# Performance work log

Hardware: AMD Instinct MI355X
Metric: run time of the kernel (lower is better)

## Reference

```python
import jax, jax.numpy as jnp
import numpy as np

B, N, C = 2, 30, 320
FH = FW = 64          # feature map (latent 128 / downsample 2)
PH = PW = 32          # roi_scale output size at this level
ORIG = 128.0          # original (latent) spatial size
SCALE = 0.5           # spatial_scale = 1/downsample_rate
SR = 2                # sampling_ratio
M = N + 1             # global channel + rois


def _bilinear(img, y, x):
    # img: (C, H, W); y, x: arbitrary-shape float coords. torchvision-style:
    # zero outside [-1, H]/[ -1, W], clamp then 4-corner interp.
    H, W = img.shape[1], img.shape[2]
    valid = (y > -1.0) & (y < H) & (x > -1.0) & (x < W)
    yc = jnp.clip(y, 0.0, H - 1.0)
    xc = jnp.clip(x, 0.0, W - 1.0)
    y0 = jnp.floor(yc).astype(jnp.int32)
    x0 = jnp.floor(xc).astype(jnp.int32)
    y1 = jnp.minimum(y0 + 1, H - 1)
    x1 = jnp.minimum(x0 + 1, W - 1)
    wy = yc - y0
    wx = xc - x0
    v = (img[:, y0, x0] * (1 - wy) * (1 - wx)
         + img[:, y0, x1] * (1 - wy) * wx
         + img[:, y1, x0] * wy * (1 - wx)
         + img[:, y1, x1] * wy * wx)
    return v * valid


def _roi_align_one(img, x1, y1, bw, bh):
    # img (C,FH,FW); x1,y1,bw,bh (N,) in aligned feature coords / bin sizes
    s = (jnp.arange(PH * SR, dtype=img.dtype) + 0.5) / SR   # sub-sample offsets in bin units
    yy = y1[:, None] + s[None, :] * bh[:, None]             # (N, PH*SR)
    xx = x1[:, None] + s[None, :] * bw[:, None]             # (N, PW*SR)
    yg = jnp.broadcast_to(yy[:, :, None], (N, PH * SR, PW * SR))
    xg = jnp.broadcast_to(xx[:, None, :], (N, PH * SR, PW * SR))
    v = _bilinear(img, yg, xg)                              # (C, N, PH*SR, PW*SR)
    v = v.reshape(C, N, PH, SR, PW, SR).mean(axis=(3, 5))   # average sub-samples
    return v.transpose(1, 0, 2, 3)                          # (N, C, PH, PW)


def _roi_unpool_one(roi_imgs, x1, y1, bw, bh):
    # inverse of roi_align: paste each (C,PH,PW) roi back into its own (FH,FW) map
    ys = jnp.arange(FH, dtype=roi_imgs.dtype)
    xs = jnp.arange(FW, dtype=roi_imgs.dtype)
    ry = (ys[None, :] - y1[:, None]) / bh[:, None] - 0.5    # (N, FH) roi-grid coords
    rx = (xs[None, :] - x1[:, None]) / bw[:, None] - 0.5    # (N, FW)
    ryg = jnp.broadcast_to(ry[:, :, None], (N, FH, FW))
    rxg = jnp.broadcast_to(rx[:, None, :], (N, FH, FW))
    return jax.vmap(_bilinear)(roi_imgs, ryg, rxg)          # (N, C, FH, FW); zeros outside box


def _fuser(x, perm, w_reduce, w1, b1, w2, b2):
    # FuseWeightGenerator: x (B, M, C, H, W)
    fg = jnp.sum(x, axis=2) != 0                            # (B, M, H, W) foreground mask
    fw = jnp.einsum('bmchw,c->bmhw', x, w_reduce)           # 1x1 conv C->1, no bias
    g = fw[:, :1]
    r = fw[:, 1:][:, perm]                                  # shuffle roi channels
    gin = jnp.concatenate([g, r], axis=1)                   # (B, M, H, W)
    # ChannelGate: only the 'max' branch affects the output (original uses last channel_att_raw)
    mp = gin.max(axis=(2, 3))                               # (B, M)
    att = jax.nn.relu(mp @ w1 + b1) @ w2 + b2
    gated = gin * jax.nn.sigmoid(att)[:, :, None, None]
    inv = jnp.argsort(perm)
    fw = jnp.concatenate([gated[:, :1], gated[:, 1:][:, inv]], axis=1)
    fw = jnp.where(fg, fw, jnp.finfo(fw.dtype).min)
    w = jax.nn.softmax(fw, axis=1)[:, :, None]              # (B, M, 1, H, W)
    return jnp.sum(x * w, axis=1)                           # (B, C, H, W)


def _forward(normed_hidden_states, attn_output, instance_boxes, instance_masks, perm,
             w_reduce, w1, b1, w2, b2):
    fmap = normed_hidden_states.reshape(B, FH, FW, C).transpose(0, 3, 1, 2)  # b c h w
    boxes = instance_boxes * ORIG * SCALE - 0.5             # aligned=True feature coords
    x1, y1 = boxes[..., 0], boxes[..., 1]
    x2, y2 = boxes[..., 2], boxes[..., 3]
    bw = (x2 - x1) / PW
    bh = (y2 - y1) / PH
    roi_feats = jax.vmap(_roi_align_one)(fmap, x1, y1, bw, bh)   # (B,N,C,PH,PW)
    mask = instance_masks.astype(roi_feats.dtype)[:, :, None, None, None]
    roi_feats = roi_feats * mask                             # masked rois stay zero
    unpooled = jax.vmap(_roi_unpool_one)(roi_feats, x1, y1, bw, bh) * mask  # (B,N,C,FH,FW)
    attn_map = attn_output.reshape(B, FH, FW, C).transpose(0, 3, 1, 2)[:, None]
    x = jnp.concatenate([attn_map, unpooled], axis=1)        # (B, M, C, FH, FW)
    fused = _fuser(x, perm, w_reduce, w1, b1, w2, b2)        # (B, C, FH, FW)
    return fused.transpose(0, 2, 3, 1).reshape(B, FH * FW, C)


def setup_inputs() -> dict:
    key = jax.random.key(0)
    ks = jax.random.split(key, 10)
    nhs = jax.random.normal(ks[0], (B, FH * FW, C), dtype=jnp.float32)
    attn = jax.random.normal(ks[1], (B, FH * FW, C), dtype=jnp.float32)
    cx = jax.random.uniform(ks[2], (B, N), minval=0.25, maxval=0.75)
    cy = jax.random.uniform(ks[3], (B, N), minval=0.25, maxval=0.75)
    hw = jax.random.uniform(ks[4], (B, N, 2), minval=0.1, maxval=0.4)
    boxes = jnp.stack([cx - hw[..., 0] / 2, cy - hw[..., 1] / 2,
                       cx + hw[..., 0] / 2, cy + hw[..., 1] / 2], axis=-1)
    boxes = jnp.clip(boxes, 0.0, 1.0).astype(jnp.float32)    # normalized xyxy
    masks = jax.random.randint(ks[5], (B, N), 0, 2).astype(jnp.int32)
    perm = jax.random.permutation(ks[6], N).astype(jnp.int32)
    w_reduce = (jax.random.normal(ks[7], (C,), dtype=jnp.float32) / np.sqrt(C)).astype(jnp.float32)
    w1 = (jax.random.normal(ks[8], (M, M), dtype=jnp.float32) / np.sqrt(M)).astype(jnp.float32)
    b1 = jnp.zeros((M,), dtype=jnp.float32)
    w2 = (jax.random.normal(ks[9], (M, M), dtype=jnp.float32) / np.sqrt(M)).astype(jnp.float32)
    b2 = jnp.zeros((M,), dtype=jnp.float32)
    return {"normed_hidden_states": nhs, "attn_output": attn, "instance_boxes": boxes,
            "instance_masks": masks, "perm": perm, "w_reduce": w_reduce,
            "w1": w1, "b1": b1, "w2": w2, "b2": b2}


def reference(normed_hidden_states, attn_output, instance_boxes, instance_masks, perm,
              w_reduce, w1, b1, w2, b2):
    return _forward(normed_hidden_states, attn_output, instance_boxes, instance_masks, perm,
                    w_reduce, w1, b1, w2, b2)
```

## Files before the change

kernel.cpp:

```cpp
#include <hip/hip_runtime.h>
#include <hip/hip_bf16.h>

#define NB 2
#define NN 30
#define NC 320
#define NM 31
#define HW 4096
#define FMIN_F (-3.40282346638528859812e+38f)

typedef float nfloat4 __attribute__((ext_vector_type(4)));

#define OFF_ASUM   0
#define OFF_AWRED  8192
#define OFF_RS     16384
#define OFF_RW     77824
#define OFF_MP     139264
#define WS_FLOATS  139328
#define ROIF_BYTE  557312

#define GRID_ROIF (NB * NN * 128)
#define GRID_RED  1639

__device__ __forceinline__ void get_box(const float* boxes, int b, int n,
                                        float& x1, float& y1, float& bw, float& bh) {
    const float* p = boxes + (b * NN + n) * 4;
    float X1 = p[0] * 64.0f - 0.5f;
    float Y1 = p[1] * 64.0f - 0.5f;
    float X2 = p[2] * 64.0f - 0.5f;
    float Y2 = p[3] * 64.0f - 0.5f;
    x1 = X1; y1 = Y1;
    bw = (X2 - X1) / 32.0f;
    bh = (Y2 - Y1) / 32.0f;
}

__device__ __forceinline__ unsigned short f2bf(float f) {
    __hip_bfloat16 h = __float2bfloat16(f);
    return *reinterpret_cast<unsigned short*>(&h);
}
__device__ __forceinline__ unsigned pack2(float a, float b) {
    return (unsigned)f2bf(a) | ((unsigned)f2bf(b) << 16);
}
__device__ __forceinline__ float blo(unsigned u) { return __uint_as_float(u << 16); }
__device__ __forceinline__ float bhi(unsigned u) { return __uint_as_float(u & 0xffff0000u); }

__device__ __forceinline__ unsigned encf(float f) {
    unsigned u = __float_as_uint(f);
    return (u & 0x80000000u) ? ~u : (u | 0x80000000u);
}
__device__ __forceinline__ float decf(unsigned e) {
    unsigned u = (e & 0x80000000u) ? (e & 0x7fffffffu) : ~e;
    return __uint_as_float(u);
}

__device__ void do_roifeat(int blk, const float* __restrict__ nhs,
                           const float* __restrict__ boxes,
                           const int* __restrict__ masks,
                           const float* __restrict__ wred,
                           float* __restrict__ ws,
                           unsigned* __restrict__ roif,
                           float* wsm , int* bsm ,
                           float* partS , float* partW ) {
    int bn = blk >> 7;
    int n = bn % NN;
    int b = bn / NN;
    if (masks[b * NN + n] == 0) return;
    int tid = threadIdx.x;
    float x1, y1, bw, bh;
    get_box(boxes, b, n, x1, y1, bw, bh);

    if (tid < 8) {
        int cell = blk * 8 + tid;
        int q = cell & 31;
        int p = (cell >> 5) & 31;
        float W[9] = {0.f,0.f,0.f,0.f,0.f,0.f,0.f,0.f,0.f};
        float wys[4], wxs[4];
        int iy0s[4], ix0s[4];
        int iymin = 64, ixmin = 64;
#pragma unroll
        for (int s_ = 0; s_ < 4; s_++) {
            int di = s_ >> 1, dj = s_ & 1;
            float y = y1 + ((float)p + 0.25f + 0.5f * (float)di) * bh;
            float x = x1 + ((float)q + 0.25f + 0.5f * (float)dj) * bw;
            float yc = fminf(fmaxf(y, 0.0f), 63.0f);
            float xc = fminf(fmaxf(x, 0.0f), 63.0f);
            int iy0 = (int)floorf(yc), ix0 = (int)floorf(xc);
            wys[s_] = yc - (float)iy0;
            wxs[s_] = xc - (float)ix0;
            iy0s[s_] = iy0; ix0s[s_] = ix0;
            iymin = min(iymin, iy0); ixmin = min(ixmin, ix0);
        }
#pragma unroll
        for (int s_ = 0; s_ < 4; s_++) {
            float wy = wys[s_], wx = wxs[s_];
            int dy = iy0s[s_] - iymin;
            int dx = ix0s[s_] - ixmin;
            bool yt = (iy0s[s_] == 63);
            bool xt = (ix0s[s_] == 63);
            float ay0 = yt ? 1.0f : (1.0f - wy);
            float ay1 = yt ? 0.0f : wy;
            float ax0 = xt ? 1.0f : (1.0f - wx);
            float ax1 = xt ? 0.0f : wx;
            float r0 = dy ? 0.0f : ay0;
            float r1 = dy ? ay0  : ay1;
            float r2 = dy ? ay1  : 0.0f;
            float c0 = dx ? 0.0f : ax0;
            float c1 = dx ? ax0  : ax1;
            float c2 = dx ? ax1  : 0.0f;
            W[0] += r0 * c0; W[1] += r0 * c1; W[2] += r0 * c2;
            W[3] += r1 * c0; W[4] += r1 * c1; W[5] += r1 * c2;
            W[6] += r2 * c0; W[7] += r2 * c1; W[8] += r2 * c2;
        }
#pragma unroll
        for (int k = 0; k < 9; k++) wsm[tid * 9 + k] = W[k] * 0.25f;
        bsm[tid] = iymin * 64 + ixmin;
    }
    __syncthreads();

    int cid = tid / 40;
    int v = tid - cid * 40;
    int cell = blk * 8 + cid;
    const float4* fb4 = (const float4*)(nhs + (size_t)b * HW * NC);
    int base = bsm[cid];
    float4 acc0 = make_float4(0.f, 0.f, 0.f, 0.f);
    float4 acc1 = make_float4(0.f, 0.f, 0.f, 0.f);
#pragma unroll
    for (int i = 0; i < 3; i++) {
#pragma unroll
        for (int j = 0; j < 3; j++) {
            float w = wsm[cid * 9 + i * 3 + j];
            if (w != 0.0f) {
                int off = (base + i * 64 + j) * 80 + v * 2;
                float4 f0 = fb4[off];
                float4 f1 = fb4[off + 1];
                acc0.x += w * f0.x; acc0.y += w * f0.y;
                acc0.z += w * f0.z; acc0.w += w * f0.w;
                acc1.x += w * f1.x; acc1.y += w * f1.y;
                acc1.z += w * f1.z; acc1.w += w * f1.w;
            }
        }
    }
    uint4 pk;
    pk.x = pack2(acc0.x, acc0.y);
    pk.y = pack2(acc0.z, acc0.w);
    pk.z = pack2(acc1.x, acc1.y);
    pk.w = pack2(acc1.z, acc1.w);
    ((uint4*)roif)[(size_t)cell * 40 + v] = pk;

    const float4* w4 = (const float4*)wred;
    float4 wv0 = w4[v * 2];
    float4 wv1 = w4[v * 2 + 1];
    partS[tid] = acc0.x + acc0.y + acc0.z + acc0.w + acc1.x + acc1.y + acc1.z + acc1.w;
    partW[tid] = acc0.x * wv0.x + acc0.y * wv0.y + acc0.z * wv0.z + acc0.w * wv0.w
               + acc1.x * wv1.x + acc1.y * wv1.y + acc1.z * wv1.z + acc1.w * wv1.w;
    __syncthreads();
    if (tid < 8) {
        float ss = 0.f, ww = 0.f;
#pragma unroll 8
        for (int k = 0; k < 40; k++) {
            ss += partS[tid * 40 + k];
            ww += partW[tid * 40 + k];
        }
        int c2 = blk * 8 + tid;
        ws[OFF_RS + c2] = ss;
        ws[OFF_RW + c2] = ww;
    }
}

__device__ void do_reduce(int rblk, const float* __restrict__ attn,
                          const float* __restrict__ wred, float* __restrict__ ws) {
    int wave = threadIdx.x >> 6;
    int lane = threadIdx.x & 63;
    int row = rblk * 5 + wave;
    if (row >= NB * HW) return;
    const float4* a4 = (const float4*)(attn + (size_t)row * NC);
    const float4* w4 = (const float4*)wred;
    float4 wv = w4[lane];
    float4 av = a4[lane];
    float s_a = av.x + av.y + av.z + av.w;
    float w_a = av.x * wv.x + av.y * wv.y + av.z * wv.z + av.w * wv.w;
    if (lane < 16) {
        float4 wv2 = w4[lane + 64];
        float4 av2 = a4[lane + 64];
        s_a += av2.x + av2.y + av2.z + av2.w;
        w_a += av2.x * wv2.x + av2.y * wv2.y + av2.z * wv2.z + av2.w * wv2.w;
    }
#pragma unroll
    for (int off = 32; off > 0; off >>= 1) {
        s_a += __shfl_down(s_a, off, 64);
        w_a += __shfl_down(w_a, off, 64);
    }
    if (lane == 0) {
        ws[OFF_ASUM + row]  = s_a;
        ws[OFF_AWRED + row] = w_a;
    }
}

__global__ void k_stage1(const float* __restrict__ nhs, const float* __restrict__ attn,
                         const float* __restrict__ boxes, const int* __restrict__ masks,
                         const float* __restrict__ wred, float* __restrict__ ws,
                         unsigned* __restrict__ roif) {
    __shared__ float wsm[72];
    __shared__ int bsm[8];
    __shared__ float partS[320], partW[320];
    int blk = blockIdx.x;
    if (blk < GRID_ROIF) {
        do_roifeat(blk, nhs, boxes, masks, wred, ws, roif, wsm, bsm, partS, partW);
    } else {
        do_reduce(blk - GRID_ROIF, attn, wred, ws);
    }
}

__global__ void k_fwmax(const float* __restrict__ boxes, const int* __restrict__ masks,
                        float* __restrict__ ws) {
    __shared__ float rwsm[1024];
    __shared__ float red[4];
    int tid = threadIdx.x;
    int bm = blockIdx.x;
    unsigned* MP = (unsigned*)(ws + OFF_MP);

    if (bm >= NB * NN) {
        int b = bm - NB * NN;
        const float* aw = ws + OFF_AWRED + b * HW;
        float lm = FMIN_F;
        for (int i = tid; i < HW; i += 256) lm = fmaxf(lm, aw[i]);
#pragma unroll
        for (int off = 32; off > 0; off >>= 1)
            lm = fmaxf(lm, __shfl_down(lm, off, 64));
        if ((tid & 63) == 0) red[tid >> 6] = lm;
        __syncthreads();
        if (tid == 0) {
            float mx = fmaxf(fmaxf(red[0], red[1]), fmaxf(red[2], red[3]));
            MP[b * NM] = encf(mx);
        }
        return;
    }

    int b = bm / NN, n = bm % NN;
    if (masks[b * NN + n] == 0) {
        if (tid == 0) MP[b * NM + 1 + n] = encf(0.0f);
        return;
    }
    const float* rw = ws + OFF_RW + (b * NN + n) * 1024;
    for (int i = tid; i < 1024; i += 256) rwsm[i] = rw[i];
    float x1, y1, bw, bh;
    get_box(boxes, b, n, x1, y1, bw, bh);
    __syncthreads();

    int h0  = max(0, (int)floorf(y1 - 0.5f * bh) - 1);
    int h1  = min(63, (int)ceilf(y1 + 32.5f * bh) + 1);
    int wq0 = max(0, (int)floorf(x1 - 0.5f * bw) - 1);
    int wq1 = min(63, (int)ceilf(x1 + 32.5f * bw) + 1);
    int Wd = wq1 - wq0 + 1;
    int tot = Wd * (h1 - h0 + 1);
    float lm = FMIN_F;
    for (int i = tid; i < tot; i += 256) {
        int h  = h0 + i / Wd;
        int wp = wq0 + i % Wd;
        float ry = ((float)h - y1) / bh - 0.5f;
        float rx = ((float)wp - x1) / bw - 0.5f;
        if (ry > -1.0f && ry < 32.0f && rx > -1.0f && rx < 32.0f) {
            float yc = fminf(fmaxf(ry, 0.0f), 31.0f);
            float xc = fminf(fmaxf(rx, 0.0f), 31.0f);
            int iy0 = (int)floorf(yc), ix0 = (int)floorf(xc);
            int iy1 = min(iy0 + 1, 31), ix1 = min(ix0 + 1, 31);
            float wy = yc - (float)iy0, wx = xc - (float)ix0;
            float fwv = (1.f - wy) * (1.f - wx) * rwsm[iy0 * 32 + ix0]
                      + (1.f - wy) * wx        * rwsm[iy0 * 32 + ix1]
                      + wy * (1.f - wx)        * rwsm[iy1 * 32 + ix0]
                      + wy * wx                * rwsm[iy1 * 32 + ix1];
            lm = fmaxf(lm, fwv);
        }
    }
#pragma unroll
    for (int off = 32; off > 0; off >>= 1)
        lm = fmaxf(lm, __shfl_down(lm, off, 64));
    if ((tid & 63) == 0) red[tid >> 6] = lm;
    __syncthreads();
    if (tid == 0) {
        float mx = fmaxf(fmaxf(red[0], red[1]), fmaxf(red[2], red[3]));
        MP[b * NM + 1 + n] = encf(fmaxf(mx, 0.0f));
    }
}

__global__ void k_final(const float* __restrict__ attn, const float* __restrict__ boxes,
                        const int* __restrict__ masks, const int* __restrict__ perm,
                        const float* __restrict__ w1, const float* __restrict__ b1,
                        const float* __restrict__ w2, const float* __restrict__ b2,
                        const float* __restrict__ ws, const unsigned* __restrict__ roif,
                        float* __restrict__ out) {
    __shared__ float mpg[NM], hb[NM], scal[32], wbuf[8][32];
    __shared__ int acnt[8];
    __shared__ unsigned char alist[8][NN];
    int t = threadIdx.x;
    int idx0 = blockIdx.x * 8;
    int b = idx0 >> 12;

    if (t < 8) acnt[t] = 0;
    if (t < NM) {
        unsigned e = ((const unsigned*)(ws + OFF_MP))[b * NM + ((t == 0) ? 0 : 1 + perm[t - 1])];
        mpg[t] = decf(e);
    }
    __syncthreads();
    if (t < NM) {
        float a = b1[t];
#pragma unroll
        for (int k = 0; k < NM; k++) a += mpg[k] * w1[k * NM + t];
        hb[t] = fmaxf(a, 0.0f);
    }
    __syncthreads();
    if (t < NM) {
        float a = b2[t];
#pragma unroll
        for (int k = 0; k < NM; k++) a += hb[k] * w2[k * NM + t];
        float sig = 1.0f / (1.0f + expf(-a));
        if (t == 0) scal[0] = sig;
        else        scal[1 + perm[t - 1]] = sig;
    }
    __syncthreads();

    if (t < 256) {
        int pg = t >> 5, m = t & 31;
        int pix = (idx0 + pg) & 4095;
        float zz = FMIN_F;
        if (m == 0) {
            float fwv = ws[OFF_AWRED + b * HW + pix];
            bool fg = (ws[OFF_ASUM + b * HW + pix] != 0.0f);
            zz = fg ? fwv * scal[0] : FMIN_F;
        } else if (m < NM) {
            int n = m - 1;
            if (masks[b * NN + n]) {
                float x1, y1, bw, bh;
                get_box(boxes, b, n, x1, y1, bw, bh);
                int h = pix >> 6, wp = pix & 63;
                float ry = ((float)h - y1) / bh - 0.5f;
                float rx = ((float)wp - x1) / bw - 0.5f;
                bool valid = (ry > -1.0f) && (ry < 32.0f) && (rx > -1.0f) && (rx < 32.0f);
                if (valid) {
                    float yc = fminf(fmaxf(ry, 0.0f), 31.0f);
                    float xc = fminf(fmaxf(rx, 0.0f), 31.0f);
                    int iy0 = (int)floorf(yc), ix0 = (int)floorf(xc);
                    int iy1 = min(iy0 + 1, 31), ix1 = min(ix0 + 1, 31);
                    float wy = yc - (float)iy0, wx = xc - (float)ix0;
                    float w00 = (1.f - wy) * (1.f - wx), w01 = (1.f - wy) * wx;
                    float w10 = wy * (1.f - wx), w11 = wy * wx;
                    const float* rw = ws + OFF_RW + (b * NN + n) * 1024;
                    const float* rs = ws + OFF_RS + (b * NN + n) * 1024;
                    float fwv = w00 * rw[iy0 * 32 + ix0] + w01 * rw[iy0 * 32 + ix1]
                              + w10 * rw[iy1 * 32 + ix0] + w11 * rw[iy1 * 32 + ix1];
                    float su  = w00 * rs[iy0 * 32 + ix0] + w01 * rs[iy0 * 32 + ix1]
                              + w10 * rs[iy1 * 32 + ix0] + w11 * rs[iy1 * 32 + ix1];
                    if (su != 0.0f) zz = fwv * scal[m];
                }
            }
        }
        float mx = zz;
#pragma unroll
        for (int off = 16; off > 0; off >>= 1)
            mx = fmaxf(mx, __shfl_xor(mx, off, 64));
        float e = (m < NM) ? expf(zz - mx) : 0.0f;
        float s = e;
#pragma unroll
        for (int off = 16; off > 0; off >>= 1)
            s += __shfl_xor(s, off, 64);
        if (m < NM) {
            float w = e / s;
            wbuf[pg][m] = w;
            if (m >= 1 && w != 0.0f) {
                int pos = atomicAdd(&acnt[pg], 1);
                alist[pg][pos] = (unsigned char)(m - 1);
            }
        }
    }
    __syncthreads();

    int pid = t / 40;
    int v = t - pid * 40;
    int idx = idx0 + pid;
    int pix = idx & 4095;
    int h = pix >> 6, wp = pix & 63;
    float w0 = wbuf[pid][0];
    const float4* at4 = (const float4*)attn;
    float4 a0 = at4[(size_t)idx * 80 + v * 2];
    float4 a1 = at4[(size_t)idx * 80 + v * 2 + 1];
    float4 acc0, acc1;
    acc0.x = a0.x * w0; acc0.y = a0.y * w0; acc0.z = a0.z * w0; acc0.w = a0.w * w0;
    acc1.x = a1.x * w0; acc1.y = a1.y * w0; acc1.z = a1.z * w0; acc1.w = a1.w * w0;
    const uint4* r4 = (const uint4*)roif;
    int na = acnt[pid];
    for (int k = 0; k < na; k++) {
        int n = alist[pid][k];
        float wn = wbuf[pid][n + 1];
        float x1, y1, bw, bh;
        get_box(boxes, b, n, x1, y1, bw, bh);
        float ry = ((float)h - y1) / bh - 0.5f;
        float rx = ((float)wp - x1) / bw - 0.5f;
        float yc = fminf(fmaxf(ry, 0.0f), 31.0f);
        float xc = fminf(fmaxf(rx, 0.0f), 31.0f);
        int iy0 = (int)floorf(yc), ix0 = (int)floorf(xc);
        int iy1 = min(iy0 + 1, 31), ix1 = min(ix0 + 1, 31);
        float wy = yc - (float)iy0, wx = xc - (float)ix0;
        float w00 = (1.f - wy) * (1.f - wx) * wn, w01 = (1.f - wy) * wx * wn;
        float w10 = wy * (1.f - wx) * wn, w11 = wy * wx * wn;
        size_t base = ((size_t)(b * NN + n)) << 10;
        uint4 U00 = r4[(base + iy0 * 32 + ix0) * 40 + v];
        uint4 U01 = r4[(base + iy0 * 32 + ix1) * 40 + v];
        uint4 U10 = r4[(base + iy1 * 32 + ix0) * 40 + v];
        uint4 U11 = r4[(base + iy1 * 32 + ix1) * 40 + v];
        acc0.x += w00 * blo(U00.x) + w01 * blo(U01.x) + w10 * blo(U10.x) + w11 * blo(U11.x);
        acc0.y += w00 * bhi(U00.x) + w01 * bhi(U01.x) + w10 * bhi(U10.x) + w11 * bhi(U11.x);
        acc0.z += w00 * blo(U00.y) + w01 * blo(U01.y) + w10 * blo(U10.y) + w11 * blo(U11.y);
        acc0.w += w00 * bhi(U00.y) + w01 * bhi(U01.y) + w10 * bhi(U10.y) + w11 * bhi(U11.y);
        acc1.x += w00 * blo(U00.z) + w01 * blo(U01.z) + w10 * blo(U10.z) + w11 * blo(U11.z);
        acc1.y += w00 * bhi(U00.z) + w01 * bhi(U01.z) + w10 * bhi(U10.z) + w11 * bhi(U11.z);
        acc1.z += w00 * blo(U00.w) + w01 * blo(U01.w) + w10 * blo(U10.w) + w11 * blo(U11.w);
        acc1.w += w00 * bhi(U00.w) + w01 * bhi(U01.w) + w10 * bhi(U10.w) + w11 * bhi(U11.w);
    }
    nfloat4 nv0 = { acc0.x, acc0.y, acc0.z, acc0.w };
    nfloat4 nv1 = { acc1.x, acc1.y, acc1.z, acc1.w };
    __builtin_nontemporal_store(nv0, ((nfloat4*)out) + (size_t)idx * 80 + v * 2);
    __builtin_nontemporal_store(nv1, ((nfloat4*)out) + (size_t)idx * 80 + v * 2 + 1);
}

extern "C" void kernel_launch(void* const* d_in, const int* in_sizes, int n_in,
                              void* d_out, int out_size, void* d_ws, size_t ws_size,
                              hipStream_t stream) {
    const float* nhs   = (const float*)d_in[0];
    const float* attn  = (const float*)d_in[1];
    const float* boxes = (const float*)d_in[2];
    const int*   masks = (const int*)d_in[3];
    const int*   perm  = (const int*)d_in[4];
    const float* wred  = (const float*)d_in[5];
    const float* w1    = (const float*)d_in[6];
    const float* b1    = (const float*)d_in[7];
    const float* w2    = (const float*)d_in[8];
    const float* b2    = (const float*)d_in[9];
    float* out = (float*)d_out;
    float* ws = (float*)d_ws;
    unsigned* roif = (unsigned*)((char*)d_ws + ROIF_BYTE);

    k_stage1<<<GRID_ROIF + GRID_RED, 320, 0, stream>>>(nhs, attn, boxes, masks, wred, ws, roif);
    k_fwmax<<<NB * NN + NB, 256, 0, stream>>>(boxes, masks, ws);
    k_final<<<NB * HW / 8, 320, 0, stream>>>(attn, boxes, masks, perm, w1, b1, w2, b2, ws, roif, out);
}
```

Baseline: 119.6 us.

## Drop materialized ROI feature maps; compose align+unpool weights directly on nhs

Removes the bf16 ROI-aligned feature buffer (B*N*1024 cells x 320 channels). The per-ROI channel sum and weighted sum are now computed from per-pixel reductions of nhs, since the reduction is linear, so only a 64x64 scalar grid needs resampling. In the final kernel the roi_align and unpool bilinear weights are composed into a separable 4x4 stencil applied to nhs directly. This removes a large write and read of intermediate data and the bf16 rounding, at the cost of up to 16 instead of 4 gathers per active ROI per pixel in the final pass.

Result: slower. 123.5 us (+3.3%).

```diff
diff --git a/kernel.cpp b/kernel.cpp
--- a/kernel.cpp
+++ b/kernel.cpp
@@ -1,5 +1,4 @@
 #include <hip/hip_runtime.h>
-#include <hip/hip_bf16.h>
 
 #define NB 2
 #define NN 30
@@ -12,14 +11,13 @@
 
 #define OFF_ASUM   0
 #define OFF_AWRED  8192
-#define OFF_RS     16384
-#define OFF_RW     77824
-#define OFF_MP     139264
-#define WS_FLOATS  139328
-#define ROIF_BYTE  557312
-
-#define GRID_ROIF (NB * NN * 128)
-#define GRID_RED  1639
+#define OFF_GS     16384
+#define OFF_GW     24576
+#define OFF_RS     32768
+#define OFF_RW     94208
+#define OFF_MP     155648
+
+#define GRID_RED 3277
 
 __device__ __forceinline__ void get_box(const float* boxes, int b, int n,
                                         float& x1, float& y1, float& bw, float& bh) {
@@ -33,16 +31,6 @@
     bh = (Y2 - Y1) / 32.0f;
 }
 
-__device__ __forceinline__ unsigned short f2bf(float f) {
-    __hip_bfloat16 h = __float2bfloat16(f);
-    return *reinterpret_cast<unsigned short*>(&h);
-}
-__device__ __forceinline__ unsigned pack2(float a, float b) {
-    return (unsigned)f2bf(a) | ((unsigned)f2bf(b) << 16);
-}
-__device__ __forceinline__ float blo(unsigned u) { return __uint_as_float(u << 16); }
-__device__ __forceinline__ float bhi(unsigned u) { return __uint_as_float(u & 0xffff0000u); }
-
 __device__ __forceinline__ unsigned encf(float f) {
     unsigned u = __float_as_uint(f);
     return (u & 0x80000000u) ? ~u : (u | 0x80000000u);
@@ -52,26 +40,92 @@
     return __uint_as_float(u);
 }
 
-__device__ void do_roifeat(int blk, const float* __restrict__ nhs,
-                           const float* __restrict__ boxes,
-                           const int* __restrict__ masks,
-                           const float* __restrict__ wred,
-                           float* __restrict__ ws,
-                           unsigned* __restrict__ roif,
-                           float* wsm , int* bsm ,
-                           float* partS , float* partW ) {
-    int bn = blk >> 7;
-    int n = bn % NN;
-    int b = bn / NN;
-    if (masks[b * NN + n] == 0) return;
+__global__ void k_reduce(const float* __restrict__ nhs, const float* __restrict__ attn,
+                         const float* __restrict__ wred, float* __restrict__ ws) {
+    int wave = threadIdx.x >> 6;
+    int lane = threadIdx.x & 63;
+    int row = blockIdx.x * 5 + wave;
+    if (row >= 2 * NB * HW) return;
+    const float* src;
+    float *d0, *d1;
+    if (row < NB * HW) {
+        src = attn + (size_t)row * NC;
+        d0 = ws + OFF_ASUM + row;
+        d1 = ws + OFF_AWRED + row;
+    } else {
+        int r = row - NB * HW;
+        src = nhs + (size_t)r * NC;
+        d0 = ws + OFF_GS + r;
+        d1 = ws + OFF_GW + r;
+    }
+    const float4* a4 = (const float4*)src;
+    const float4* w4 = (const float4*)wred;
+    float4 wv = w4[lane];
+    float4 av = a4[lane];
+    float s_a = av.x + av.y + av.z + av.w;
+    float w_a = av.x * wv.x + av.y * wv.y + av.z * wv.z + av.w * wv.w;
+    if (lane < 16) {
+        float4 wv2 = w4[lane + 64];
+        float4 av2 = a4[lane + 64];
+        s_a += av2.x + av2.y + av2.z + av2.w;
+        w_a += av2.x * wv2.x + av2.y * wv2.y + av2.z * wv2.z + av2.w * wv2.w;
+    }
+#pragma unroll
+    for (int off = 32; off > 0; off >>= 1) {
+        s_a += __shfl_down(s_a, off, 64);
+        w_a += __shfl_down(w_a, off, 64);
+    }
+    if (lane == 0) {
+        d0[0] = s_a;
+        d1[0] = w_a;
+    }
+}
+
+__global__ void k_grids(const float* __restrict__ boxes, const int* __restrict__ masks,
+                        float* __restrict__ ws) {
+    __shared__ float gsm[4096], gwm[4096];
+    __shared__ float rwsm[1024];
+    __shared__ float red[4];
     int tid = threadIdx.x;
+    int bm = blockIdx.x;
+    unsigned* MP = (unsigned*)(ws + OFF_MP);
+
+    if (bm >= NB * NN) {
+        int b = bm - NB * NN;
+        const float* aw = ws + OFF_AWRED + b * HW;
+        float lm = FMIN_F;
+        for (int i = tid; i < HW; i += 256) lm = fmaxf(lm, aw[i]);
+#pragma unroll
+        for (int off = 32; off > 0; off >>= 1)
+            lm = fmaxf(lm, __shfl_down(lm, off, 64));
+        if ((tid & 63) == 0) red[tid >> 6] = lm;
+        __syncthreads();
+        if (tid == 0) {
+            float mx = fmaxf(fmaxf(red[0], red[1]), fmaxf(red[2], red[3]));
+            MP[b * NM] = encf(mx);
+        }
+        return;
+    }
+
+    int b = bm / NN, n = bm % NN;
+    if (masks[b * NN + n] == 0) {
+        if (tid == 0) MP[b * NM + 1 + n] = encf(0.0f);
+        return;
+    }
+    const float* gs = ws + OFF_GS + b * HW;
+    const float* gw = ws + OFF_GW + b * HW;
+    for (int i = tid; i < 4096; i += 256) {
+        gsm[i] = gs[i];
+        gwm[i] = gw[i];
+    }
     float x1, y1, bw, bh;
     get_box(boxes, b, n, x1, y1, bw, bh);
-
-    if (tid < 8) {
-        int cell = blk * 8 + tid;
-        int q = cell & 31;
-        int p = (cell >> 5) & 31;
+    __syncthreads();
+
+    float* RS = ws + OFF_RS + (b * NN + n) * 1024;
+    float* RW = ws + OFF_RW + (b * NN + n) * 1024;
+    for (int c = tid; c < 1024; c += 256) {
+        int q = c & 31, p = c >> 5;
         float W[9] = {0.f,0.f,0.f,0.f,0.f,0.f,0.f,0.f,0.f};
         float wys[4], wxs[4];
         int iy0s[4], ix0s[4];
@@ -110,140 +164,21 @@
             W[3] += r1 * c0; W[4] += r1 * c1; W[5] += r1 * c2;
             W[6] += r2 * c0; W[7] += r2 * c1; W[8] += r2 * c2;
         }
-#pragma unroll
-        for (int k = 0; k < 9; k++) wsm[tid * 9 + k] = W[k] * 0.25f;
-        bsm[tid] = iymin * 64 + ixmin;
-    }
-    __syncthreads();
-
-    int cid = tid / 40;
-    int v = tid - cid * 40;
-    int cell = blk * 8 + cid;
-    const float4* fb4 = (const float4*)(nhs + (size_t)b * HW * NC);
-    int base = bsm[cid];
-    float4 acc0 = make_float4(0.f, 0.f, 0.f, 0.f);
-    float4 acc1 = make_float4(0.f, 0.f, 0.f, 0.f);
-#pragma unroll
-    for (int i = 0; i < 3; i++) {
-#pragma unroll
-        for (int j = 0; j < 3; j++) {
-            float w = wsm[cid * 9 + i * 3 + j];
-            if (w != 0.0f) {
-                int off = (base + i * 64 + j) * 80 + v * 2;
-                float4 f0 = fb4[off];
-                float4 f1 = fb4[off + 1];
-                acc0.x += w * f0.x; acc0.y += w * f0.y;
-                acc0.z += w * f0.z; acc0.w += w * f0.w;
-                acc1.x += w * f1.x; acc1.y += w * f1.y;
-                acc1.z += w * f1.z; acc1.w += w * f1.w;
+        int base = iymin * 64 + ixmin;
+        float ss = 0.f, ww = 0.f;
+#pragma unroll
+        for (int k = 0; k < 9; k++) {
+            if (W[k] != 0.0f) {
+                float wk = W[k] * 0.25f;
+                int off = base + (k / 3) * 64 + (k % 3);
+                ss += wk * gsm[off];
+                ww += wk * gwm[off];
             }
         }
-    }
-    uint4 pk;
-    pk.x = pack2(acc0.x, acc0.y);
-    pk.y = pack2(acc0.z, acc0.w);
-    pk.z = pack2(acc1.x, acc1.y);
-    pk.w = pack2(acc1.z, acc1.w);
-    ((uint4*)roif)[(size_t)cell * 40 + v] = pk;
-
-    const float4* w4 = (const float4*)wred;
-    float4 wv0 = w4[v * 2];
-    float4 wv1 = w4[v * 2 + 1];
-    partS[tid] = acc0.x + acc0.y + acc0.z + acc0.w + acc1.x + acc1.y + acc1.z + acc1.w;
-    partW[tid] = acc0.x * wv0.x + acc0.y * wv0.y + acc0.z * wv0.z + acc0.w * wv0.w
-               + acc1.x * wv1.x + acc1.y * wv1.y + acc1.z * wv1.z + acc1.w * wv1.w;
-    __syncthreads();
-    if (tid < 8) {
-        float ss = 0.f, ww = 0.f;
-#pragma unroll 8
-        for (int k = 0; k < 40; k++) {
-            ss += partS[tid * 40 + k];
-            ww += partW[tid * 40 + k];
-        }
-        int c2 = blk * 8 + tid;
-        ws[OFF_RS + c2] = ss;
-        ws[OFF_RW + c2] = ww;
-    }
-}
-
-__device__ void do_reduce(int rblk, const float* __restrict__ attn,
-                          const float* __restrict__ wred, float* __restrict__ ws) {
-    int wave = threadIdx.x >> 6;
-    int lane = threadIdx.x & 63;
-    int row = rblk * 5 + wave;
-    if (row >= NB * HW) return;
-    const float4* a4 = (const float4*)(attn + (size_t)row * NC);
-    const float4* w4 = (const float4*)wred;
-    float4 wv = w4[lane];
-    float4 av = a4[lane];
-    float s_a = av.x + av.y + av.z + av.w;
-    float w_a = av.x * wv.x + av.y * wv.y + av.z * wv.z + av.w * wv.w;
-    if (lane < 16) {
-        float4 wv2 = w4[lane + 64];
-        float4 av2 = a4[lane + 64];
-        s_a += av2.x + av2.y + av2.z + av2.w;
-        w_a += av2.x * wv2.x + av2.y * wv2.y + av2.z * wv2.z + av2.w * wv2.w;
-    }
-#pragma unroll
-    for (int off = 32; off > 0; off >>= 1) {
-        s_a += __shfl_down(s_a, off, 64);
-        w_a += __shfl_down(w_a, off, 64);
-    }
-    if (lane == 0) {
-        ws[OFF_ASUM + row]  = s_a;
-        ws[OFF_AWRED + row] = w_a;
-    }
-}
-
-__global__ void k_stage1(const float* __restrict__ nhs, const float* __restrict__ attn,
-                         const float* __restrict__ boxes, const int* __restrict__ masks,
-                         const float* __restrict__ wred, float* __restrict__ ws,
-                         unsigned* __restrict__ roif) {
-    __shared__ float wsm[72];
-    __shared__ int bsm[8];
-    __shared__ float partS[320], partW[320];
-    int blk = blockIdx.x;
-    if (blk < GRID_ROIF) {
-        do_roifeat(blk, nhs, boxes, masks, wred, ws, roif, wsm, bsm, partS, partW);
-    } else {
-        do_reduce(blk - GRID_ROIF, attn, wred, ws);
-    }
-}
-
-__global__ void k_fwmax(const float* __restrict__ boxes, const int* __restrict__ masks,
-                        float* __restrict__ ws) {
-    __shared__ float rwsm[1024];
-    __shared__ float red[4];
-    int tid = threadIdx.x;
-    int bm = blockIdx.x;
-    unsigned* MP = (unsigned*)(ws + OFF_MP);
-
-    if (bm >= NB * NN) {
-        int b = bm - NB * NN;
-        const float* aw = ws + OFF_AWRED + b * HW;
-        float lm = FMIN_F;
-        for (int i = tid; i < HW; i += 256) lm = fmaxf(lm, aw[i]);
-#pragma unroll
-        for (int off = 32; off > 0; off >>= 1)
-            lm = fmaxf(lm, __shfl_down(lm, off, 64));
-        if ((tid & 63) == 0) red[tid >> 6] = lm;
-        __syncthreads();
-        if (tid == 0) {
-            float mx = fmaxf(fmaxf(red[0], red[1]), fmaxf(red[2], red[3]));
-            MP[b * NM] = encf(mx);
-        }
-        return;
-    }
-
-    int b = bm / NN, n = bm % NN;
-    if (masks[b * NN + n] == 0) {
-        if (tid == 0) MP[b * NM + 1 + n] = encf(0.0f);
-        return;
-    }
-    const float* rw = ws + OFF_RW + (b * NN + n) * 1024;
-    for (int i = tid; i < 1024; i += 256) rwsm[i] = rw[i];
-    float x1, y1, bw, bh;
-    get_box(boxes, b, n, x1, y1, bw, bh);
+        RS[c] = ss;
+        RW[c] = ww;
+        rwsm[c] = ww;
+    }
     __syncthreads();
 
     int h0  = max(0, (int)floorf(y1 - 0.5f * bh) - 1);
@@ -282,12 +217,12 @@
     }
 }
 
-__global__ void k_final(const float* __restrict__ attn, const float* __restrict__ boxes,
-                        const int* __restrict__ masks, const int* __restrict__ perm,
+__global__ void k_final(const float* __restrict__ nhs, const float* __restrict__ attn,
+                        const float* __restrict__ boxes, const int* __restrict__ masks,
+                        const int* __restrict__ perm,
                         const float* __restrict__ w1, const float* __restrict__ b1,
                         const float* __restrict__ w2, const float* __restrict__ b2,
-                        const float* __restrict__ ws, const unsigned* __restrict__ roif,
-                        float* __restrict__ out) {
+                        const float* __restrict__ ws, float* __restrict__ out) {
     __shared__ float mpg[NM], hb[NM], scal[32], wbuf[8][32];
     __shared__ int acnt[8];
     __shared__ unsigned char alist[8][NN];
@@ -385,7 +320,7 @@
     float4 acc0, acc1;
     acc0.x = a0.x * w0; acc0.y = a0.y * w0; acc0.z = a0.z * w0; acc0.w = a0.w * w0;
     acc1.x = a1.x * w0; acc1.y = a1.y * w0; acc1.z = a1.z * w0; acc1.w = a1.w * w0;
-    const uint4* r4 = (const uint4*)roif;
+    const float4* fb4 = (const float4*)(nhs + (size_t)b * HW * NC);
     int na = acnt[pid];
     for (int k = 0; k < na; k++) {
         int n = alist[pid][k];
@@ -398,22 +333,60 @@
         float xc = fminf(fmaxf(rx, 0.0f), 31.0f);
         int iy0 = (int)floorf(yc), ix0 = (int)floorf(xc);
         int iy1 = min(iy0 + 1, 31), ix1 = min(ix0 + 1, 31);
-        float wy = yc - (float)iy0, wx = xc - (float)ix0;
-        float w00 = (1.f - wy) * (1.f - wx) * wn, w01 = (1.f - wy) * wx * wn;
-        float w10 = wy * (1.f - wx) * wn, w11 = wy * wx * wn;
-        size_t base = ((size_t)(b * NN + n)) << 10;
-        uint4 U00 = r4[(base + iy0 * 32 + ix0) * 40 + v];
-        uint4 U01 = r4[(base + iy0 * 32 + ix1) * 40 + v];
-        uint4 U10 = r4[(base + iy1 * 32 + ix0) * 40 + v];
-        uint4 U11 = r4[(base + iy1 * 32 + ix1) * 40 + v];
-        acc0.x += w00 * blo(U00.x) + w01 * blo(U01.x) + w10 * blo(U10.x) + w11 * blo(U11.x);
-        acc0.y += w00 * bhi(U00.x) + w01 * bhi(U01.x) + w10 * bhi(U10.x) + w11 * bhi(U11.x);
-        acc0.z += w00 * blo(U00.y) + w01 * blo(U01.y) + w10 * blo(U10.y) + w11 * blo(U11.y);
-        acc0.w += w00 * bhi(U00.y) + w01 * bhi(U01.y) + w10 * bhi(U10.y) + w11 * bhi(U11.y);
-        acc1.x += w00 * blo(U00.z) + w01 * blo(U01.z) + w10 * blo(U10.z) + w11 * blo(U11.z);
-        acc1.y += w00 * bhi(U00.z) + w01 * bhi(U01.z) + w10 * bhi(U10.z) + w11 * bhi(U11.z);
-        acc1.z += w00 * blo(U00.w) + w01 * blo(U01.w) + w10 * blo(U10.w) + w11 * blo(U11.w);
-        acc1.w += w00 * bhi(U00.w) + w01 * bhi(U01.w) + w10 * bhi(U10.w) + w11 * bhi(U11.w);
+        float fy = yc - (float)iy0, fx = xc - (float)ix0;
+
+        float ya00 = fminf(fmaxf(y1 + ((float)iy0 + 0.25f) * bh, 0.f), 63.f);
+        float ya01 = fminf(fmaxf(y1 + ((float)iy0 + 0.75f) * bh, 0.f), 63.f);
+        float ya10 = fminf(fmaxf(y1 + ((float)iy1 + 0.25f) * bh, 0.f), 63.f);
+        float ya11 = fminf(fmaxf(y1 + ((float)iy1 + 0.75f) * bh, 0.f), 63.f);
+        float xa00 = fminf(fmaxf(x1 + ((float)ix0 + 0.25f) * bw, 0.f), 63.f);
+        float xa01 = fminf(fmaxf(x1 + ((float)ix0 + 0.75f) * bw, 0.f), 63.f);
+        float xa10 = fminf(fmaxf(x1 + ((float)ix1 + 0.25f) * bw, 0.f), 63.f);
+        float xa11 = fminf(fmaxf(x1 + ((float)ix1 + 0.75f) * bw, 0.f), 63.f);
+        int rb = (int)floorf(ya00);
+        int cb = (int)floorf(xa00);
+        float wyv[4] = {0.f,0.f,0.f,0.f};
+        float wxv[4] = {0.f,0.f,0.f,0.f};
+        float cy0 = 0.5f * (1.0f - fy), cy1 = 0.5f * fy;
+        float cx0 = 0.5f * (1.0f - fx), cx1 = 0.5f * fx;
+        {
+            int i; float f;
+            i = (int)floorf(ya00); f = ya00 - (float)i;
+            wyv[i - rb] += cy0 * (1.f - f); wyv[min(i + 1, 63) - rb] += cy0 * f;
+            i = (int)floorf(ya01); f = ya01 - (float)i;
+            wyv[i - rb] += cy0 * (1.f - f); wyv[min(i + 1, 63) - rb] += cy0 * f;
+            i = (int)floorf(ya10); f = ya10 - (float)i;
+            wyv[i - rb] += cy1 * (1.f - f); wyv[min(i + 1, 63) - rb] += cy1 * f;
+            i = (int)floorf(ya11); f = ya11 - (float)i;
+            wyv[i - rb] += cy1 * (1.f - f); wyv[min(i + 1, 63) - rb] += cy1 * f;
+            i = (int)floorf(xa00); f = xa00 - (float)i;
+            wxv[i - cb] += cx0 * (1.f - f); wxv[min(i + 1, 63) - cb] += cx0 * f;
+            i = (int)floorf(xa01); f = xa01 - (float)i;
+            wxv[i - cb] += cx0 * (1.f - f); wxv[min(i + 1, 63) - cb] += cx0 * f;
+            i = (int)floorf(xa10); f = xa10 - (float)i;
+            wxv[i - cb] += cx1 * (1.f - f); wxv[min(i + 1, 63) - cb] += cx1 * f;
+            i = (int)floorf(xa11); f = xa11 - (float)i;
+            wxv[i - cb] += cx1 * (1.f - f); wxv[min(i + 1, 63) - cb] += cx1 * f;
+        }
+#pragma unroll
+        for (int r = 0; r < 4; r++) {
+            float wy = wyv[r];
+            if (wy == 0.f) continue;
+            int rowoff = (rb + r) * 64 + cb;
+#pragma unroll
+            for (int cc = 0; cc < 4; cc++) {
+                float wgt = wy * wxv[cc];
+                if (wgt == 0.f) continue;
+                wgt *= wn;
+                int off = (rowoff + cc) * 80 + v * 2;
+                float4 f0 = fb4[off];
+                float4 f1 = fb4[off + 1];
+                acc0.x += wgt * f0.x; acc0.y += wgt * f0.y;
+                acc0.z += wgt * f0.z; acc0.w += wgt * f0.w;
+                acc1.x += wgt * f1.x; acc1.y += wgt * f1.y;
+                acc1.z += wgt * f1.z; acc1.w += wgt * f1.w;
+            }
+        }
     }
     nfloat4 nv0 = { acc0.x, acc0.y, acc0.z, acc0.w };
     nfloat4 nv1 = { acc1.x, acc1.y, acc1.z, acc1.w };
@@ -436,9 +409,9 @@
     const float* b2    = (const float*)d_in[9];
     float* out = (float*)d_out;
     float* ws = (float*)d_ws;
-    unsigned* roif = (unsigned*)((char*)d_ws + ROIF_BYTE);
-
-    k_stage1<<<GRID_ROIF + GRID_RED, 320, 0, stream>>>(nhs, attn, boxes, masks, wred, ws, roif);
-    k_fwmax<<<NB * NN + NB, 256, 0, stream>>>(boxes, masks, ws);
-    k_final<<<NB * HW / 8, 320, 0, stream>>>(attn, boxes, masks, perm, w1, b1, w2, b2, ws, roif, out);
-}
+
+    k_reduce<<<GRID_RED, 320, 0, stream>>>(nhs, attn, wred, ws);
+    k_grids<<<NB * NN + NB, 256, 0, stream>>>(boxes, masks, ws);
+    k_final<<<NB * HW / 8, 320, 0, stream>>>(nhs, attn, boxes, masks, perm,
+                                             w1, b1, w2, b2, ws, out);
+}
```
